# Optimization experiments

Measured on AMD Instinct MI355X. Metric: run time of the kernel, lower is better.

## Reference

```python
import jax, jax.numpy as jnp
import numpy as np
from jax import lax

IN_DIM = 512
MID = IN_DIM // 2          # 256
HEADS = 8
B, H, W = 16, 64, 64
BN_EPS = 1e-5
NORM_EPS = 1e-12


def setup_inputs() -> dict:
    key = jax.random.key(0)
    ks = jax.random.split(key, 16)
    r = lambda k, shape, s=0.02: jax.random.normal(k, shape, dtype=jnp.float32) * s
    return {
        "x": jax.random.normal(ks[0], (B, IN_DIM, H, W), dtype=jnp.float32),
        "reduce_w": r(ks[1], (MID, IN_DIM)),
        "reduce_b": jnp.zeros((MID,), jnp.float32),
        "dw_w": r(ks[2], (MID, 1, 3, 3), 0.1),
        "dw_b": jnp.zeros((MID,), jnp.float32),
        "bn_gamma": jnp.ones((MID,), jnp.float32),
        "bn_beta": jnp.zeros((MID,), jnp.float32),
        "bn_mean": r(ks[3], (MID,), 0.1),
        "bn_var": jnp.ones((MID,), jnp.float32),
        "gate_w1": r(ks[4], (MID // 8, MID)),
        "gate_b1": jnp.zeros((MID // 8,), jnp.float32),
        "gate_w2": r(ks[5], (MID, MID // 8)),
        "gate_b2": jnp.zeros((MID,), jnp.float32),
        "temperature": jnp.ones((HEADS, 1, 1), jnp.float32),
        "post_w": r(ks[6], (IN_DIM, 2 * MID)),
        "post_b": jnp.zeros((IN_DIM,), jnp.float32),
    }


def reference(x, reduce_w, reduce_b, dw_w, dw_b, bn_gamma, bn_beta, bn_mean, bn_var,
              gate_w1, gate_b1, gate_w2, gate_b2, temperature, post_w, post_b):
    Bsz, C, Hh, Ww = x.shape
    # reduce (1x1 conv) -> depthwise 3x3 -> BN (eval stats) -> ReLU
    xr = jnp.einsum('bchw,oc->bohw', x, reduce_w) + reduce_b[:, None, None]
    xr = lax.conv_general_dilated(xr, dw_w, (1, 1), 'SAME',
                                  feature_group_count=MID,
                                  dimension_numbers=('NCHW', 'OIHW', 'NCHW'))
    xr = xr + dw_b[:, None, None]
    inv = bn_gamma / jnp.sqrt(bn_var + BN_EPS)
    xr = (xr - bn_mean[:, None, None]) * inv[:, None, None] + bn_beta[:, None, None]
    xr = jax.nn.relu(xr)

    # FFT channel attention
    fft_feat = jnp.fft.fft2(xr, norm='ortho')              # complex64 [B,MID,H,W]
    HWn = Hh * Ww
    qkv = fft_feat.reshape(Bsz, HEADS, MID // HEADS, HWn)  # b h c n (complex)
    nrm = jnp.sqrt(jnp.sum(jnp.abs(qkv) ** 2, axis=-1, keepdims=True))
    qn = qkv / jnp.maximum(nrm, NORM_EPS)                  # L2-normalize complex rows
    attn = jnp.einsum('bhcn,bhdn->bhcd', qn, qn)           # complex, no conjugate (matches torch)
    attn = attn * temperature                               # [h,1,1] real broadcast
    attn = jax.nn.softmax(attn.real, axis=-1)
    out = jnp.einsum('bhcd,bhdn->bhcn', attn, qkv.real)
    out = out.reshape(Bsz, MID, Hh, Ww).astype(jnp.complex64)
    out = jnp.fft.ifft2(out, norm='ortho').real

    # SE gate + frequency-domain recombine (default fft norm, as in torch)
    g = jnp.mean(xr, axis=(-2, -1))                         # [B,MID]
    g = jax.nn.relu(g @ gate_w1.T + gate_b1)
    g = jax.nn.sigmoid(g @ gate_w2.T + gate_b2)
    gated = g[:, :, None, None] * xr
    fwm = jnp.fft.ifft2(fft_feat * jnp.fft.fft2(gated)).real

    fused = jnp.concatenate([out, fwm], axis=1)             # [B,2*MID,H,W]
    y = jnp.einsum('bchw,oc->bohw', fused, post_w) + post_b[:, None, None] + x
    return y
```

## Files before the change

kernel.cpp:

```cpp
#include <hip/hip_runtime.h>
#include <math.h>

#define BATCH 16
#define CIN   512
#define MID   256
#define HW    4096
#define HEADS 8
#define CH    32
#define KSPL  8
#define PI2   6.2831853071795864769f
#define RT2H  0.70710678118654752440f

typedef __attribute__((ext_vector_type(8))) short short8;
typedef __attribute__((ext_vector_type(4))) float floatx4;
typedef __attribute__((ext_vector_type(16))) float floatx16;

__device__ inline unsigned short f2b(float f) {
  union { float f; unsigned int u; } v; v.f = f;
  unsigned int u = v.u;
  unsigned int r = (u + 0x7fffu + ((u >> 16) & 1u)) >> 16;
  return (unsigned short)r;
}

__device__ __forceinline__ int swidx(int r, int n) {
  return (r << 6) + (n ^ (r & 15));
}

__device__ __forceinline__ void cmadd(float2& a, const float2 x,
                                      const float wr, const float wi) {
  a.x = fmaf(x.x, wr, a.x); a.x = fmaf(-x.y, wi, a.x);
  a.y = fmaf(x.x, wi, a.y); a.y = fmaf(x.y, wr, a.y);
}

template<int SGN, int AXIS>
__device__ __forceinline__ void dft64_pass(float2* __restrict__ buf,
                                           const float2* __restrict__ tw,
                                           const int tid)
{
  constexpr float W8R[8] = {1.f, RT2H, 0.f, -RT2H, -1.f, -RT2H, 0.f, RT2H};
  constexpr float W8I[8] = {0.f, RT2H, 1.f, RT2H, 0.f, -RT2H, -1.f, -RT2H};
  const int line = tid & 63;
  const int wv = tid >> 6;
  float2 xa[2][8];

  #pragma unroll
  for (int t = 0; t < 2; ++t) {
    const int b = wv + (t << 2);
    #pragma unroll
    for (int a = 0; a < 8; ++a) {
      const int i = (a << 3) + b;
      xa[t][a] = buf[AXIS ? swidx(line, i) : swidx(i, line)];
    }
  }
  __syncthreads();
  #pragma unroll
  for (int t = 0; t < 2; ++t) {
    const int b = wv + (t << 2);
    #pragma unroll
    for (int d = 0; d < 8; ++d) {
      float2 y = make_float2(0.f, 0.f);
      #pragma unroll
      for (int a = 0; a < 8; ++a) {
        const int j = (a * d) & 7;
        cmadd(y, xa[t][a], W8R[j], (float)SGN * W8I[j]);
      }
      const float2 tb = tw[(b * d) & 63];
      float2 z;
      z.x = y.x * tb.x - y.y * tb.y;
      z.y = y.x * tb.y + y.y * tb.x;
      const int i = (b << 3) + d;
      buf[AXIS ? swidx(line, i) : swidx(i, line)] = z;
    }
  }
  __syncthreads();

  #pragma unroll
  for (int t = 0; t < 2; ++t) {
    const int d = wv + (t << 2);
    #pragma unroll
    for (int b = 0; b < 8; ++b) {
      const int i = (b << 3) + d;
      xa[t][b] = buf[AXIS ? swidx(line, i) : swidx(i, line)];
    }
  }
  __syncthreads();
  #pragma unroll
  for (int t = 0; t < 2; ++t) {
    const int d = wv + (t << 2);
    #pragma unroll
    for (int c = 0; c < 8; ++c) {
      float2 s = make_float2(0.f, 0.f);
      #pragma unroll
      for (int b = 0; b < 8; ++b) {
        const int j = (b * c) & 7;
        cmadd(s, xa[t][b], W8R[j], (float)SGN * W8I[j]);
      }
      const int i = (c << 3) + d;
      buf[AXIS ? swidx(line, i) : swidx(i, line)] = s;
    }
  }
  __syncthreads();
}

__global__ __launch_bounds__(256) void k_castw(
    const float* __restrict__ rw, const float* __restrict__ pw,
    unsigned short* __restrict__ rwB, unsigned short* __restrict__ pwB)
{
  int i = blockIdx.x * 256 + threadIdx.x;
  if (i < MID * CIN) rwB[i] = f2b(rw[i]);
  if (i < CIN * 2 * MID) pwB[i] = f2b(pw[i]);
}

#define LDT 40

__global__ __launch_bounds__(256) void k_gemm_red(
    const unsigned short* __restrict__ A, const float* __restrict__ Bg0,
    const float* __restrict__ bias, float* __restrict__ out)
{
  __shared__ __align__(16) short As[128 * LDT];
  __shared__ __align__(16) short Bs[128 * LDT];
  const int tid = threadIdx.x;
  const int n0 = blockIdx.x << 7;
  const int m0 = blockIdx.y << 7;
  const int b  = blockIdx.z;
  const int lane = tid & 63, wave = tid >> 6;
  const int wm = (wave >> 1) << 6, wn = (wave & 1) << 6;
  const int l16 = lane & 15, quad = lane >> 4;
  const float* Bg = Bg0 + (size_t)b * CIN * HW;
  floatx4 acc[4][4] = {};
  for (int k0 = 0; k0 < CIN; k0 += 32) {
    #pragma unroll
    for (int l = tid; l < 512; l += 256) {
      int m = l >> 2, ko = (l & 3) << 3;
      *(uint4*)&As[m * LDT + ko] = *(const uint4*)&A[(size_t)(m0 + m) * CIN + k0 + ko];
    }
    #pragma unroll
    for (int it = 0; it < 16; ++it) {
      int l = tid + (it << 8);
      int k = l >> 7, n = l & 127;
      Bs[n * LDT + k] = (short)f2b(Bg[(size_t)(k0 + k) * HW + n0 + n]);
    }
    __syncthreads();
    short8 af[4], bf[4];
    #pragma unroll
    for (int mi = 0; mi < 4; ++mi)
      af[mi] = *(const short8*)&As[(wm + (mi << 4) + l16) * LDT + (quad << 3)];
    #pragma unroll
    for (int ni = 0; ni < 4; ++ni)
      bf[ni] = *(const short8*)&Bs[(wn + (ni << 4) + l16) * LDT + (quad << 3)];
    #pragma unroll
    for (int mi = 0; mi < 4; ++mi)
      #pragma unroll
      for (int ni = 0; ni < 4; ++ni)
        acc[mi][ni] = __builtin_amdgcn_mfma_f32_16x16x32_bf16(af[mi], bf[ni], acc[mi][ni], 0, 0, 0);
    __syncthreads();
  }
  #pragma unroll
  for (int mi = 0; mi < 4; ++mi)
    #pragma unroll
    for (int reg = 0; reg < 4; ++reg) {
      int m = m0 + wm + (mi << 4) + (quad << 2) + reg;
      float bv = bias[m];
      size_t base = ((size_t)b * MID + m) * HW + n0 + wn + l16;
      #pragma unroll
      for (int ni = 0; ni < 4; ++ni)
        out[base + (ni << 4)] = acc[mi][ni][reg] + bv;
    }
}

__global__ __launch_bounds__(256) void k_gemm_post(
    const unsigned short* __restrict__ A, const float* __restrict__ fftf,
    const float* __restrict__ bias, const float* __restrict__ x,
    float* __restrict__ y)
{
  __shared__ __align__(16) short As[128 * LDT];
  __shared__ __align__(16) short Bs[128 * LDT];
  const int tid = threadIdx.x;
  const int n0 = blockIdx.x << 7;
  const int m0 = blockIdx.y << 7;
  const int b  = blockIdx.z;
  const int lane = tid & 63, wave = tid >> 6;
  const int wm = (wave >> 1) << 6, wn = (wave & 1) << 6;
  const int l16 = lane & 15, quad = lane >> 4;
  floatx4 acc[4][4] = {};
  for (int k0 = 0; k0 < 2 * MID; k0 += 32) {
    #pragma unroll
    for (int l = tid; l < 512; l += 256) {
      int m = l >> 2, ko = (l & 3) << 3;
      *(uint4*)&As[m * LDT + ko] = *(const uint4*)&A[(size_t)(m0 + m) * (2 * MID) + k0 + ko];
    }
    #pragma unroll
    for (int it = 0; it < 16; ++it) {
      int l = tid + (it << 8);
      int k = l >> 7, n = l & 127;
      int cidx = k0 + k;
      const unsigned short* row = (const unsigned short*)
          (fftf + (size_t)(b * MID + (cidx & 255)) * (2 * HW) + ((cidx < MID) ? HW : 0));
      Bs[n * LDT + k] = (short)row[n0 + n];
    }
    __syncthreads();
    short8 af[4], bf[4];
    #pragma unroll
    for (int mi = 0; mi < 4; ++mi)
      af[mi] = *(const short8*)&As[(wm + (mi << 4) + l16) * LDT + (quad << 3)];
    #pragma unroll
    for (int ni = 0; ni < 4; ++ni)
      bf[ni] = *(const short8*)&Bs[(wn + (ni << 4) + l16) * LDT + (quad << 3)];
    #pragma unroll
    for (int mi = 0; mi < 4; ++mi)
      #pragma unroll
      for (int ni = 0; ni < 4; ++ni)
        acc[mi][ni] = __builtin_amdgcn_mfma_f32_16x16x32_bf16(af[mi], bf[ni], acc[mi][ni], 0, 0, 0);
    __syncthreads();
  }
  #pragma unroll
  for (int mi = 0; mi < 4; ++mi)
    #pragma unroll
    for (int reg = 0; reg < 4; ++reg) {
      int m = m0 + wm + (mi << 4) + (quad << 2) + reg;
      float bv = bias[m];
      size_t base = ((size_t)b * CIN + m) * HW + n0 + wn + l16;
      #pragma unroll
      for (int ni = 0; ni < 4; ++ni)
        y[base + (ni << 4)] = acc[mi][ni][reg] + bv + x[base + (ni << 4)];
    }
}

__global__ __launch_bounds__(256) void k_dwbn(
    const float* __restrict__ in, const float* __restrict__ dww,
    const float* __restrict__ dwb, const float* __restrict__ gamma,
    const float* __restrict__ beta, const float* __restrict__ mean,
    const float* __restrict__ var, float* __restrict__ out,
    float* __restrict__ g0)
{
  __shared__ float pl[HW];
  __shared__ float red[256];
  const int p = blockIdx.x;
  const int c = p & (MID - 1);
  const int tid = threadIdx.x;
  const float* ip = in + (size_t)p * HW;
  for (int l = tid; l < HW; l += 256) pl[l] = ip[l];
  float wreg[9];
  #pragma unroll
  for (int i = 0; i < 9; ++i) wreg[i] = dww[c * 9 + i];
  const float bconv = dwb[c];
  const float inv = gamma[c] * rsqrtf(var[c] + 1e-5f);
  const float mu = mean[c], bt = beta[c];
  __syncthreads();
  float lsum = 0.f;
  float* op = out + (size_t)p * HW;
  for (int l = tid; l < HW; l += 256) {
    int y = l >> 6, xx0 = l & 63;
    float s = bconv;
    #pragma unroll
    for (int ky = 0; ky < 3; ++ky) {
      int yy = y + ky - 1;
      if (yy < 0 || yy >= 64) continue;
      #pragma unroll
      for (int kx = 0; kx < 3; ++kx) {
        int xx = xx0 + kx - 1;
        if (xx < 0 || xx >= 64) continue;
        s = fmaf(pl[(yy << 6) + xx], wreg[ky * 3 + kx], s);
      }
    }
    s = (s - mu) * inv + bt;
    s = fmaxf(s, 0.f);
    op[l] = s;
    lsum += s;
  }
  red[tid] = lsum;
  __syncthreads();
  for (int st = 128; st > 0; st >>= 1) {
    if (tid < st) red[tid] += red[tid + st];
    __syncthreads();
  }
  if (tid == 0) g0[p] = red[0] * (1.f / HW);
}

__global__ __launch_bounds__(256) void k_gate(
    const float* __restrict__ g0, const float* __restrict__ w1,
    const float* __restrict__ b1, const float* __restrict__ w2,
    const float* __restrict__ b2, float* __restrict__ g)
{
  __shared__ float gs[MID];
  __shared__ float hs[32];
  const int b = blockIdx.x;
  const int tid = threadIdx.x;
  gs[tid] = g0[b * MID + tid];
  __syncthreads();
  if (tid < 32) {
    float s = b1[tid];
    for (int c = 0; c < MID; ++c) s = fmaf(gs[c], w1[tid * MID + c], s);
    hs[tid] = fmaxf(s, 0.f);
  }
  __syncthreads();
  float s = b2[tid];
  #pragma unroll
  for (int j = 0; j < 32; ++j) s = fmaf(hs[j], w2[tid * 32 + j], s);
  g[b * MID + tid] = 1.f / (1.f + expf(-s));
}

__global__ __launch_bounds__(256) void k_fft_fwd(
    const float* __restrict__ in, float* __restrict__ outf,
    float* __restrict__ Nbuf)
{
  __shared__ float2 buf[64 * 64];
  __shared__ float2 tw[64];
  __shared__ float red[256];
  const int tid = threadIdx.x;
  const int p = blockIdx.x;
  if (tid < 64) {
    float ang = -PI2 * (float)tid * (1.f / 64.f);
    tw[tid] = make_float2(cosf(ang), sinf(ang));
  }
  const float* ip = in + (size_t)p * HW;
  for (int l = tid; l < HW; l += 256)
    buf[swidx(l >> 6, l & 63)] = make_float2(ip[l], 0.f);
  __syncthreads();
  dft64_pass<-1, 0>(buf, tw, tid);
  dft64_pass<-1, 1>(buf, tw, tid);
  float2* op = (float2*)(outf + (size_t)p * (2 * HW));
  float lsum = 0.f;
  for (int l = tid; l < HW; l += 256) {
    float2 v = buf[swidx(l >> 6, l & 63)];
    float vx = v.x * (1.f / 64.f), vy = v.y * (1.f / 64.f);
    op[l] = make_float2(vx, vy);
    lsum = fmaf(vx, vx, fmaf(vy, vy, lsum));
  }
  red[tid] = lsum;
  __syncthreads();
  for (int st = 128; st > 0; st >>= 1) {
    if (tid < st) red[tid] += red[tid + st];
    __syncthreads();
  }
  if (tid == 0) Nbuf[p] = red[0];
}

__global__ __launch_bounds__(256) void k_attn_s(
    const float* __restrict__ fftf, float* __restrict__ Sbuf)
{
  __shared__ float red[4 * 1024];
  const int bh = blockIdx.y;
  const int ks = blockIdx.x;
  const int b = bh >> 3, h = bh & 7;
  const int tid = threadIdx.x;
  const int lane = tid & 63, wave = tid >> 6;
  const int r  = lane & 31;
  const int hi = lane >> 5;
  const float* rowp = fftf + (size_t)(b * MID + h * CH + r) * (2 * HW)
                    + (size_t)ks * (2 * HW / KSPL) + wave * (2 * HW / KSPL / 4)
                    + (hi << 3);
  floatx16 acc = {};
  #pragma unroll
  for (int st = 0; st < (2 * HW / KSPL / 4) / 16; ++st) {
    float4 f0 = *(const float4*)(rowp + st * 16);
    float4 f1 = *(const float4*)(rowp + st * 16 + 4);
    short8 a;
    a[0] = (short)f2b(f0.x); a[1] = (short)f2b(f0.y);
    a[2] = (short)f2b(f0.z); a[3] = (short)f2b(f0.w);
    a[4] = (short)f2b(f1.x); a[5] = (short)f2b(f1.y);
    a[6] = (short)f2b(f1.z); a[7] = (short)f2b(f1.w);
    uint4 av = *(uint4*)&a;
    uint4 bv = make_uint4(av.x ^ 0x80000000u, av.y ^ 0x80000000u,
                          av.z ^ 0x80000000u, av.w ^ 0x80000000u);
    short8 bn = *(short8*)&bv;
    acc = __builtin_amdgcn_mfma_f32_32x32x16_bf16(a, bn, acc, 0, 0, 0);
  }
  #pragma unroll
  for (int i = 0; i < 16; ++i) {
    const int row = (i & 3) + ((i >> 2) << 3) + (hi << 2);
    red[wave * 1024 + row * 32 + r] = acc[i];
  }
  __syncthreads();
  float* Sp = Sbuf + ((size_t)bh * KSPL + ks) * 1024;
  #pragma unroll
  for (int e = tid; e < 1024; e += 256)
    Sp[e] = red[e] + red[1024 + e] + red[2048 + e] + red[3072 + e];
}

__global__ __launch_bounds__(64) void k_attn_sm(
    const float* __restrict__ Sbuf, const float* __restrict__ Nbuf,
    const float* __restrict__ temp, float* __restrict__ Pbuf)
{
  const int bh = blockIdx.x;
  const int h = bh & 7;
  const int tid = threadIdx.x;
  if (tid < 32) {
    float nc = fmaxf(sqrtf(Nbuf[bh * 32 + tid]), 1e-12f);
    float tmp = temp[h];
    const float* Sp = Sbuf + (size_t)bh * (KSPL * 1024) + tid * 32;
    float vals[32];
    float vmax = -1e30f;
    #pragma unroll
    for (int d = 0; d < 32; ++d) {
      float s = 0.f;
      #pragma unroll
      for (int ksx = 0; ksx < KSPL; ++ksx) s += Sp[ksx * 1024 + d];
      float nd = fmaxf(sqrtf(Nbuf[bh * 32 + d]), 1e-12f);
      float v = s / (nc * nd) * tmp;
      vals[d] = v;
      vmax = fmaxf(vmax, v);
    }
    float sum = 0.f;
    #pragma unroll
    for (int d = 0; d < 32; ++d) {
      float e = expf(vals[d] - vmax);
      vals[d] = e;
      sum += e;
    }
    float rinv = 1.f / sum;
    float* Pp = Pbuf + (size_t)bh * 1024 + tid * 32;
    #pragma unroll
    for (int d = 0; d < 32; ++d) Pp[d] = vals[d] * rinv;
  }
}

__global__ __launch_bounds__(256) void k_attn_o(
    const float* __restrict__ fftf, const float* __restrict__ Pbuf,
    float* __restrict__ outw)
{
  const int bh = blockIdx.y;
  const int n0 = blockIdx.x << 9;
  const int b = bh >> 3, h = bh & 7;
  const float2* Q = (const float2*)fftf + ((size_t)b * MID + (size_t)h * CH) * HW;
  __shared__ float P[1024];
  __shared__ float Lr[32 * 514];
  const int tid = threadIdx.x;
  for (int l = tid; l < 1024; l += 256) P[l] = Pbuf[(size_t)bh * 1024 + l];
  for (int l = tid; l < 32 * 512; l += 256) {
    int r = l >> 9, nn = l & 511;
    Lr[r * 514 + nn] = Q[(size_t)r * HW + n0 + nn].x;
  }
  __syncthreads();
  const float2* Lr2 = (const float2*)Lr;
  const float4* P4 = (const float4*)P;
  float* orow = outw + ((size_t)b * MID + (size_t)h * CH) * HW + n0;
  #pragma unroll 4
  for (int c = 0; c < 32; ++c) {
    float s0 = 0.f, s1 = 0.f;
    #pragma unroll
    for (int j = 0; j < 8; ++j) {
      float4 pv = P4[c * 8 + j];
      int d = j << 2;
      float2 v0 = Lr2[(d + 0) * 257 + tid];
      float2 v1 = Lr2[(d + 1) * 257 + tid];
      float2 v2 = Lr2[(d + 2) * 257 + tid];
      float2 v3 = Lr2[(d + 3) * 257 + tid];
      s0 = fmaf(pv.x, v0.x, s0); s1 = fmaf(pv.x, v0.y, s1);
      s0 = fmaf(pv.y, v1.x, s0); s1 = fmaf(pv.y, v1.y, s1);
      s0 = fmaf(pv.z, v2.x, s0); s1 = fmaf(pv.z, v2.y, s1);
      s0 = fmaf(pv.w, v3.x, s0); s1 = fmaf(pv.w, v3.y, s1);
    }
    ((float2*)(orow + (size_t)c * HW))[tid] = make_float2(s0, s1);
  }
}

__global__ __launch_bounds__(256) void k_ifft_re(
    const float* __restrict__ in, float* __restrict__ fftf)
{
  __shared__ float2 buf[64 * 64];
  __shared__ float2 tw[64];
  const int tid = threadIdx.x;
  const int p = blockIdx.x;
  if (tid < 64) {
    float ang = -PI2 * (float)tid * (1.f / 64.f);
    tw[tid] = make_float2(cosf(ang), sinf(ang));
  }
  const float* ip = in + (size_t)p * HW;
  for (int l = tid; l < HW; l += 256)
    buf[swidx(l >> 6, l & 63)] = make_float2(ip[l], 0.f);
  __syncthreads();
  dft64_pass<-1, 0>(buf, tw, tid);
  dft64_pass<-1, 1>(buf, tw, tid);
  unsigned short* op = (unsigned short*)(fftf + (size_t)p * (2 * HW) + HW);
  for (int l = tid; l < HW; l += 256) {
    float2 v = buf[swidx(l >> 6, l & 63)];
    op[l] = f2b(v.x * (1.f / 64.f));
  }
}

__global__ __launch_bounds__(256) void k_fwm(
    float* __restrict__ fftf, const float* __restrict__ g)
{
  __shared__ float2 buf[64 * 64];
  __shared__ float2 tw[64];
  const int tid = threadIdx.x;
  const int p = blockIdx.x;
  if (tid < 64) {
    float ang = PI2 * (float)tid * (1.f / 64.f);
    tw[tid] = make_float2(cosf(ang), sinf(ang));
  }
  float* plane = fftf + (size_t)p * (2 * HW);
  const float2* F = (const float2*)plane;
  for (int l = tid; l < HW; l += 256) {
    float2 v = F[l];
    buf[swidx(l >> 6, l & 63)] = make_float2(v.x * v.x - v.y * v.y, 2.f * v.x * v.y);
  }
  __syncthreads();
  dft64_pass<1, 0>(buf, tw, tid);
  dft64_pass<1, 1>(buf, tw, tid);
  const float gg = g[p] * (1.f / 64.f);
  unsigned short* ob = (unsigned short*)plane;
  for (int l = tid; l < HW; l += 256) {
    float2 v = buf[swidx(l >> 6, l & 63)];
    ob[l] = f2b(v.x * gg);
  }
}

extern "C" void kernel_launch(void* const* d_in, const int* in_sizes, int n_in,
                              void* d_out, int out_size, void* d_ws, size_t ws_size,
                              hipStream_t stream)
{
  const float* x    = (const float*)d_in[0];
  const float* rw   = (const float*)d_in[1];
  const float* rb   = (const float*)d_in[2];
  const float* dww  = (const float*)d_in[3];
  const float* dwb  = (const float*)d_in[4];
  const float* bng  = (const float*)d_in[5];
  const float* bnb  = (const float*)d_in[6];
  const float* bnm  = (const float*)d_in[7];
  const float* bnv  = (const float*)d_in[8];
  const float* gw1  = (const float*)d_in[9];
  const float* gb1  = (const float*)d_in[10];
  const float* gw2  = (const float*)d_in[11];
  const float* gb2  = (const float*)d_in[12];
  const float* temp = (const float*)d_in[13];
  const float* pw   = (const float*)d_in[14];
  const float* pb   = (const float*)d_in[15];
  float* y = (float*)d_out;

  float* ws = (float*)d_ws;
  const size_t PL = (size_t)BATCH * MID * HW;
  float* xr   = ws;
  float* fftf = ws + PL;
  float* g0   = ws + 3 * PL;
  float* gg   = g0 + BATCH * MID;
  float* Nbuf = gg + BATCH * MID;
  unsigned short* rwB = (unsigned short*)(Nbuf + BATCH * MID);
  unsigned short* pwB = rwB + MID * CIN;
  float* Sbuf = xr;
  float* Pbuf = xr + (size_t)BATCH * HEADS * KSPL * 1024;
  float* xr0  = y;

  k_castw    <<<dim3(1024),            256, 0, stream>>>(rw, pw, rwB, pwB);
  k_gemm_red <<<dim3(32, 2, BATCH),    256, 0, stream>>>(rwB, x, rb, xr0);
  k_dwbn     <<<dim3(BATCH * MID),     256, 0, stream>>>(xr0, dww, dwb, bng, bnb, bnm, bnv, xr, g0);
  k_gate     <<<dim3(BATCH),           256, 0, stream>>>(g0, gw1, gb1, gw2, gb2, gg);
  k_fft_fwd  <<<dim3(BATCH * MID),     256, 0, stream>>>(xr, fftf, Nbuf);
  k_attn_s   <<<dim3(KSPL, BATCH * HEADS), 256, 0, stream>>>(fftf, Sbuf);
  k_attn_sm  <<<dim3(BATCH * HEADS),   64,  0, stream>>>(Sbuf, Nbuf, temp, Pbuf);
  k_attn_o   <<<dim3(8, BATCH * HEADS), 256, 0, stream>>>(fftf, Pbuf, xr0);
  k_fwm      <<<dim3(BATCH * MID),     256, 0, stream>>>(fftf, gg);
  k_ifft_re  <<<dim3(BATCH * MID),     256, 0, stream>>>(xr0, fftf);
  k_gemm_post<<<dim3(32, 4, BATCH),    256, 0, stream>>>(pwB, fftf, pb, x, y);
}
```

Measured before the change: 718.3 us.

## Double GEMM K-tile and vectorize transposed B staging with XOR-swizzled LDS

Both 1x1-conv GEMMs now stage a K-tile of 64 instead of 32, which halves the number of barrier pairs per block. The B operand was previously written to LDS one scalar short at a time with a strided transpose. It is now loaded as float2 or uint32 pairs, packed into bf16 pairs in registers, and stored as 16-byte vectors into an XOR-swizzled layout with a 144-byte row pitch to avoid bank conflicts. This cuts global load instruction count and LDS store traffic, at the cost of more shared memory per block and more complex indexing.

After: 655.9 us. -8.7%, faster.

```diff
diff --git a/kernel.cpp b/kernel.cpp
--- a/kernel.cpp
+++ b/kernel.cpp
@@ -111,14 +111,13 @@
   if (i < CIN * 2 * MID) pwB[i] = f2b(pw[i]);
 }
 
-#define LDT 40
 
 __global__ __launch_bounds__(256) void k_gemm_red(
     const unsigned short* __restrict__ A, const float* __restrict__ Bg0,
     const float* __restrict__ bias, float* __restrict__ out)
 {
-  __shared__ __align__(16) short As[128 * LDT];
-  __shared__ __align__(16) short Bs[128 * LDT];
+  __shared__ __align__(16) char As[128 * 144];
+  __shared__ __align__(16) char Bs[128 * 144];
   const int tid = threadIdx.x;
   const int n0 = blockIdx.x << 7;
   const int m0 = blockIdx.y << 7;
@@ -128,31 +127,49 @@
   const int l16 = lane & 15, quad = lane >> 4;
   const float* Bg = Bg0 + (size_t)b * CIN * HW;
   floatx4 acc[4][4] = {};
-  for (int k0 = 0; k0 < CIN; k0 += 32) {
-    #pragma unroll
-    for (int l = tid; l < 512; l += 256) {
-      int m = l >> 2, ko = (l & 3) << 3;
-      *(uint4*)&As[m * LDT + ko] = *(const uint4*)&A[(size_t)(m0 + m) * CIN + k0 + ko];
-    }
-    #pragma unroll
-    for (int it = 0; it < 16; ++it) {
+  for (int k0 = 0; k0 < CIN; k0 += 64) {
+    #pragma unroll
+    for (int it = 0; it < 4; ++it) {
       int l = tid + (it << 8);
-      int k = l >> 7, n = l & 127;
-      Bs[n * LDT + k] = (short)f2b(Bg[(size_t)(k0 + k) * HW + n0 + n]);
+      int m = l >> 3, ko = (l & 7) << 3;
+      *(uint4*)(As + m * 144 + (ko << 1)) =
+          *(const uint4*)&A[(size_t)(m0 + m) * CIN + k0 + ko];
+    }
+    #pragma unroll
+    for (int it = 0; it < 2; ++it) {
+      int id = tid + (it << 8);
+      int np = id & 63, q = id >> 6;
+      const float* r0 = Bg + (size_t)(k0 + (q << 3)) * HW + n0 + (np << 1);
+      unsigned int d0[4], d1[4];
+      #pragma unroll
+      for (int p = 0; p < 4; ++p) {
+        float2 va = *(const float2*)(r0 + (size_t)(2 * p) * HW);
+        float2 vb = *(const float2*)(r0 + (size_t)(2 * p + 1) * HW);
+        d0[p] = (unsigned int)f2b(va.x) | ((unsigned int)f2b(vb.x) << 16);
+        d1[p] = (unsigned int)f2b(va.y) | ((unsigned int)f2b(vb.y) << 16);
+      }
+      char* dst = Bs + (np << 1) * 144 + ((q ^ (np & 7)) << 4);
+      *(uint4*)dst = make_uint4(d0[0], d0[1], d0[2], d0[3]);
+      *(uint4*)(dst + 144) = make_uint4(d1[0], d1[1], d1[2], d1[3]);
     }
     __syncthreads();
-    short8 af[4], bf[4];
-    #pragma unroll
-    for (int mi = 0; mi < 4; ++mi)
-      af[mi] = *(const short8*)&As[(wm + (mi << 4) + l16) * LDT + (quad << 3)];
-    #pragma unroll
-    for (int ni = 0; ni < 4; ++ni)
-      bf[ni] = *(const short8*)&Bs[(wn + (ni << 4) + l16) * LDT + (quad << 3)];
-    #pragma unroll
-    for (int mi = 0; mi < 4; ++mi)
-      #pragma unroll
-      for (int ni = 0; ni < 4; ++ni)
-        acc[mi][ni] = __builtin_amdgcn_mfma_f32_16x16x32_bf16(af[mi], bf[ni], acc[mi][ni], 0, 0, 0);
+    #pragma unroll
+    for (int kk = 0; kk < 2; ++kk) {
+      short8 af[4], bf[4];
+      #pragma unroll
+      for (int mi = 0; mi < 4; ++mi)
+        af[mi] = *(const short8*)(As + (wm + (mi << 4) + l16) * 144 + (kk << 6) + (quad << 4));
+      #pragma unroll
+      for (int ni = 0; ni < 4; ++ni) {
+        int n = wn + (ni << 4) + l16;
+        bf[ni] = *(const short8*)(Bs + n * 144 + ((((kk << 2) + quad) ^ ((n >> 1) & 7)) << 4));
+      }
+      #pragma unroll
+      for (int mi = 0; mi < 4; ++mi)
+        #pragma unroll
+        for (int ni = 0; ni < 4; ++ni)
+          acc[mi][ni] = __builtin_amdgcn_mfma_f32_16x16x32_bf16(af[mi], bf[ni], acc[mi][ni], 0, 0, 0);
+    }
     __syncthreads();
   }
   #pragma unroll
@@ -173,8 +190,8 @@
     const float* __restrict__ bias, const float* __restrict__ x,
     float* __restrict__ y)
 {
-  __shared__ __align__(16) short As[128 * LDT];
-  __shared__ __align__(16) short Bs[128 * LDT];
+  __shared__ __align__(16) char As[128 * 144];
+  __shared__ __align__(16) char Bs[128 * 144];
   const int tid = threadIdx.x;
   const int n0 = blockIdx.x << 7;
   const int m0 = blockIdx.y << 7;
@@ -183,34 +200,52 @@
   const int wm = (wave >> 1) << 6, wn = (wave & 1) << 6;
   const int l16 = lane & 15, quad = lane >> 4;
   floatx4 acc[4][4] = {};
-  for (int k0 = 0; k0 < 2 * MID; k0 += 32) {
-    #pragma unroll
-    for (int l = tid; l < 512; l += 256) {
-      int m = l >> 2, ko = (l & 3) << 3;
-      *(uint4*)&As[m * LDT + ko] = *(const uint4*)&A[(size_t)(m0 + m) * (2 * MID) + k0 + ko];
-    }
-    #pragma unroll
-    for (int it = 0; it < 16; ++it) {
+  for (int k0 = 0; k0 < 2 * MID; k0 += 64) {
+    #pragma unroll
+    for (int it = 0; it < 4; ++it) {
       int l = tid + (it << 8);
-      int k = l >> 7, n = l & 127;
-      int cidx = k0 + k;
-      const unsigned short* row = (const unsigned short*)
-          (fftf + (size_t)(b * MID + (cidx & 255)) * (2 * HW) + ((cidx < MID) ? HW : 0));
-      Bs[n * LDT + k] = (short)row[n0 + n];
+      int m = l >> 3, ko = (l & 7) << 3;
+      *(uint4*)(As + m * 144 + (ko << 1)) =
+          *(const uint4*)&A[(size_t)(m0 + m) * (2 * MID) + k0 + ko];
+    }
+    #pragma unroll
+    for (int it = 0; it < 2; ++it) {
+      int id = tid + (it << 8);
+      int np = id & 63, q = id >> 6;
+      int c0 = k0 + (q << 3);
+      const unsigned short* bp = (const unsigned short*)
+          (fftf + (size_t)(b * MID + (c0 & 255)) * (2 * HW) + ((c0 < MID) ? HW : 0));
+      const unsigned int* bp32 = (const unsigned int*)(bp + n0) + np;
+      unsigned int d0[4], d1[4];
+      #pragma unroll
+      for (int p = 0; p < 4; ++p) {
+        unsigned int a  = bp32[(size_t)(2 * p) * (2 * HW)];
+        unsigned int bq = bp32[(size_t)(2 * p + 1) * (2 * HW)];
+        d0[p] = (a & 0xffffu) | (bq << 16);
+        d1[p] = (a >> 16) | (bq & 0xffff0000u);
+      }
+      char* dst = Bs + (np << 1) * 144 + ((q ^ (np & 7)) << 4);
+      *(uint4*)dst = make_uint4(d0[0], d0[1], d0[2], d0[3]);
+      *(uint4*)(dst + 144) = make_uint4(d1[0], d1[1], d1[2], d1[3]);
     }
     __syncthreads();
-    short8 af[4], bf[4];
-    #pragma unroll
-    for (int mi = 0; mi < 4; ++mi)
-      af[mi] = *(const short8*)&As[(wm + (mi << 4) + l16) * LDT + (quad << 3)];
-    #pragma unroll
-    for (int ni = 0; ni < 4; ++ni)
-      bf[ni] = *(const short8*)&Bs[(wn + (ni << 4) + l16) * LDT + (quad << 3)];
-    #pragma unroll
-    for (int mi = 0; mi < 4; ++mi)
-      #pragma unroll
-      for (int ni = 0; ni < 4; ++ni)
-        acc[mi][ni] = __builtin_amdgcn_mfma_f32_16x16x32_bf16(af[mi], bf[ni], acc[mi][ni], 0, 0, 0);
+    #pragma unroll
+    for (int kk = 0; kk < 2; ++kk) {
+      short8 af[4], bf[4];
+      #pragma unroll
+      for (int mi = 0; mi < 4; ++mi)
+        af[mi] = *(const short8*)(As + (wm + (mi << 4) + l16) * 144 + (kk << 6) + (quad << 4));
+      #pragma unroll
+      for (int ni = 0; ni < 4; ++ni) {
+        int n = wn + (ni << 4) + l16;
+        bf[ni] = *(const short8*)(Bs + n * 144 + ((((kk << 2) + quad) ^ ((n >> 1) & 7)) << 4));
+      }
+      #pragma unroll
+      for (int mi = 0; mi < 4; ++mi)
+        #pragma unroll
+        for (int ni = 0; ni < 4; ++ni)
+          acc[mi][ni] = __builtin_amdgcn_mfma_f32_16x16x32_bf16(af[mi], bf[ni], acc[mi][ni], 0, 0, 0);
+    }
     __syncthreads();
   }
   #pragma unroll
```
